# Optimization experiments

Measured on AMD Instinct MI355X. Metric: run time of the kernel, lower is better.

## Reference

```python
import jax, jax.numpy as jnp
import numpy as np

N = 1200          # number of mentions in the block -> NxN SDP matrix
HID = 128         # MLP hidden width
RANK = 64         # Burer-Monteiro factor rank ~ sqrt(2N)
SDP_ITERS = 100   # fixed iteration budget (original caps at 50000)
BN_EPS = 1e-5


def setup_inputs() -> dict:
    key = jax.random.key(0)
    k = jax.random.split(key, 5)
    P = N * (N - 1) // 2
    x = jax.random.normal(k[0], (P, 39), jnp.float32)
    W1 = jax.random.normal(k[1], (39, HID), jnp.float32) * (1.0 / np.sqrt(39.0))
    b1 = jnp.zeros((HID,), jnp.float32)
    gamma = jnp.ones((HID,), jnp.float32)
    beta = jnp.zeros((HID,), jnp.float32)
    W2 = jax.random.normal(k[2], (HID, 1), jnp.float32) * (1.0 / np.sqrt(float(HID)))
    b2 = jnp.zeros((1,), jnp.float32)
    V0 = jax.random.normal(k[3], (N, RANK), jnp.float32)
    return {"x": x, "W1": W1, "b1": b1, "gamma": gamma, "beta": beta,
            "W2": W2, "b2": b2, "V0": V0}


def _forward(x, W1, b1, gamma, beta, W2, b2, V0):
    # MLPLayer: Linear -> BatchNorm (batch stats) -> ReLU -> Linear(->1)
    h = x @ W1 + b1                                   # [P, HID]
    mu = h.mean(axis=0)
    var = h.var(axis=0)
    h = (h - mu) * jax.lax.rsqrt(var + BN_EPS) * gamma + beta
    h = jax.nn.relu(h)
    w = (h @ W2 + b2).reshape(-1)                     # flat edge weights [P]

    # UncompressTransformLayer: flat upper-triangle -> symmetric NxN, zero diag
    iu, ju = jnp.triu_indices(N, k=1)
    A = jnp.zeros((N, N), w.dtype).at[iu, ju].set(w)
    W = A + A.T                                       # [N, N]

    # SDPLayer: max <W, X> s.t. X PSD, diag(X)=1, X>=0 via Burer-Monteiro
    # low-rank factorization with fixed-iteration projected gradient ascent.
    V = V0 / jnp.linalg.norm(V0, axis=1, keepdims=True)
    lr = 1.0 / (jnp.linalg.norm(W) + 1e-8)

    def step(V, _):
        V = V + lr * (W @ V)
        V = V / jnp.linalg.norm(V, axis=1, keepdims=True)
        return V, None

    V, _ = jax.lax.scan(step, V, None, length=SDP_ITERS)
    X = jnp.clip(V @ V.T, 0.0, 1.0)                   # output probabilities [N, N]
    return X


def reference(x, W1, b1, gamma, beta, W2, b2, V0):
    return _forward(x, W1, b1, gamma, beta, W2, b2, V0)
```

## Files before the change

### kernel.cpp

```cpp
#include <hip/hip_runtime.h>

#define NM 1200
#define PP 719400
#define HID 128
#define RANK 64
#define SDP_ITERS 100

#define OFF_S      0
#define OFF_SUMW2  1600
#define OFF_CVEC   1664
#define OFF_W1S    1792
#define OFF_WVEC   6912
#define OFF_WMAT   726400
#define OFF_VA     2166400
#define OFF_VB     2243200

__device__ __forceinline__ float wave_reduce_sum(float v) {
#pragma unroll
    for (int o = 32; o > 0; o >>= 1) v += __shfl_xor(v, o, 64);
    return v;
}

__global__ __launch_bounds__(256) void zero_kernel(float* __restrict__ ws, int n) {
    int i = blockIdx.x * 256 + threadIdx.x;
    if (i < n) ws[i] = 0.0f;
}

#define STATS_BLOCKS 1024
#define KT 40
__global__ __launch_bounds__(256) void stats_kernel(const float* __restrict__ x,
                                                    float* __restrict__ S) {
    __shared__ __align__(8) float tile[KT * 48];
    __shared__ float Sacc[48 * 48];
    const int tid = threadIdx.x;
    for (int i = tid; i < 48 * 48; i += 256) Sacc[i] = 0.f;

    const int rpb = (PP + STATS_BLOCKS - 1) / STATS_BLOCKS;
    const int r0 = blockIdx.x * rpb;
    const int r1 = min(r0 + rpb, PP);

    const int z  = tid >> 6;
    const int ln = tid & 63;
    const int ty = ln >> 3, tx = ln & 7;

    float acc[6][6];
#pragma unroll
    for (int a = 0; a < 6; ++a)
#pragma unroll
        for (int b = 0; b < 6; ++b) acc[a][b] = 0.f;

    for (int t = r0; t < r1; t += KT) {
        const int nr = min(KT, r1 - t);
        __syncthreads();
        const float* xg = x + (size_t)t * 39;
        for (int idx = tid; idx < KT * 48; idx += 256) {
            int rr = idx / 48, cc = idx - rr * 48;
            float v = 0.f;
            if (rr < nr) {
                if (cc < 39) v = xg[rr * 39 + cc];
                else if (cc == 39) v = 1.0f;
            }
            tile[idx] = v;
        }
        __syncthreads();
#pragma unroll 2
        for (int kk = 0; kk < KT / 4; ++kk) {
            const float* row = &tile[(kk * 4 + z) * 48];
            float2 a0 = *(const float2*)(row + ty * 6);
            float2 a1 = *(const float2*)(row + ty * 6 + 2);
            float2 a2 = *(const float2*)(row + ty * 6 + 4);
            float2 b0 = *(const float2*)(row + tx * 6);
            float2 b1 = *(const float2*)(row + tx * 6 + 2);
            float2 b2 = *(const float2*)(row + tx * 6 + 4);
            float av[6] = {a0.x, a0.y, a1.x, a1.y, a2.x, a2.y};
            float bv[6] = {b0.x, b0.y, b1.x, b1.y, b2.x, b2.y};
#pragma unroll
            for (int a = 0; a < 6; ++a)
#pragma unroll
                for (int b = 0; b < 6; ++b)
                    acc[a][b] = fmaf(av[a], bv[b], acc[a][b]);
        }
    }
    __syncthreads();
#pragma unroll
    for (int a = 0; a < 6; ++a)
#pragma unroll
        for (int b = 0; b < 6; ++b)
            atomicAdd(&Sacc[(ty * 6 + a) * 48 + tx * 6 + b], acc[a][b]);
    __syncthreads();
    for (int i = tid; i < 1600; i += 256) {
        int r = i / 40, c = i - r * 40;
        atomicAdd(&S[i], Sacc[r * 48 + c]);
    }
}

__global__ __launch_bounds__(64) void bn_prep(const float* __restrict__ S,
                                              const float* __restrict__ W1,
                                              const float* __restrict__ gamma,
                                              const float* __restrict__ beta,
                                              float* __restrict__ W1s,
                                              float* __restrict__ cvec) {
    const int j = blockIdx.x;
    const int l = threadIdx.x;
    const float invP = 1.0f / (float)PP;
    float q = 0.f;
    for (int idx = l; idx < 39 * 39; idx += 64) {
        int a = idx / 39, b = idx - a * 39;
        q = fmaf(S[a * 40 + b], W1[a * HID + j] * W1[b * HID + j], q);
    }
    float s1 = (l < 39) ? (S[39 * 40 + l] * invP) * W1[l * HID + j] : 0.f;
    q = wave_reduce_sum(q);
    s1 = wave_reduce_sum(s1);
    float var = q * invP - s1 * s1;
    float scale = gamma[j] * (1.0f / sqrtf(var + 1e-5f));
    for (int a = l; a < 39; a += 64) W1s[a * HID + j] = W1[a * HID + j] * scale;
    if (l == 0) cvec[j] = -s1 * scale + beta[j];
}

__global__ __launch_bounds__(256) void mlp_kernel(const float* __restrict__ x,
                                                  const float* __restrict__ W1s,
                                                  const float* __restrict__ cvec,
                                                  const float* __restrict__ W2,
                                                  const float* __restrict__ b2,
                                                  float* __restrict__ w,
                                                  float* __restrict__ sumw2) {
    __shared__ float xt[256 * 39];
    __shared__ float red[4];
    const size_t base = (size_t)blockIdx.x * 256;
    {
        const size_t g0 = base * 39;
        const size_t gmax = (size_t)PP * 39;
        for (int idx = threadIdx.x; idx < 256 * 39; idx += 256) {
            size_t g = g0 + idx;
            xt[idx] = (g < gmax) ? x[g] : 0.f;
        }
    }
    __syncthreads();

    float xr[39];
    {
        const float* xrow = &xt[threadIdx.x * 39];
#pragma unroll
        for (int k = 0; k < 39; ++k) xr[k] = xrow[k];
    }

    float wacc = 0.f;
#pragma unroll 1
    for (int c = 0; c < 2; ++c) {
        float acc[64];
#pragma unroll
        for (int jj = 0; jj < 64; ++jj) acc[jj] = cvec[c * 64 + jj];
#pragma unroll 3
        for (int k = 0; k < 39; ++k) {
            const float xk = xr[k];
            const float* wrow = &W1s[k * HID + c * 64];
#pragma unroll
            for (int jj = 0; jj < 64; ++jj) acc[jj] = fmaf(xk, wrow[jj], acc[jj]);
        }
#pragma unroll
        for (int jj = 0; jj < 64; ++jj)
            wacc = fmaf(fmaxf(acc[jj], 0.f), W2[c * 64 + jj], wacc);
    }

    const size_t p = base + threadIdx.x;
    const float wv = wacc + b2[0];
    float sq = 0.f;
    if (p < (size_t)PP) { w[p] = wv; sq = wv * wv; }
    sq = wave_reduce_sum(sq);
    if ((threadIdx.x & 63) == 0) red[threadIdx.x >> 6] = sq;
    __syncthreads();
    if (threadIdx.x == 0) atomicAdd(sumw2, red[0] + red[1] + red[2] + red[3]);
}

__global__ __launch_bounds__(256) void buildW(const float* __restrict__ w,
                                              float* __restrict__ W) {
    __shared__ float tile[16][17];
    const int bi = blockIdx.y, bj = blockIdx.x;
    if (bi > bj) return;
    const int ty = threadIdx.x >> 4, tx = threadIdx.x & 15;
    const int i = bi * 16 + ty, j = bj * 16 + tx;
    float v = 0.f;
    if (i < j) {
        int p = i * (NM - 1) - (i * (i - 1)) / 2 + (j - i - 1);
        v = w[p];
    }
    tile[ty][tx] = v;
    __syncthreads();
    if (bi == bj) {
        float out = (i < j) ? v : ((i > j) ? tile[tx][ty] : 0.f);
        W[(size_t)i * NM + j] = out;
    } else {
        W[(size_t)i * NM + j] = v;
        W[(size_t)(bj * 16 + ty) * NM + (bi * 16 + tx)] = tile[tx][ty];
    }
}

__global__ __launch_bounds__(256) void v0norm(const float* __restrict__ V0,
                                              float* __restrict__ V) {
    const int i = blockIdx.x * 4 + (threadIdx.x >> 6);
    const int c = threadIdx.x & 63;
    float v = V0[(size_t)i * RANK + c];
    float s = wave_reduce_sum(v * v);
    V[(size_t)i * RANK + c] = v * (1.0f / sqrtf(s));
}

__global__ __launch_bounds__(512) void sdp_step(const float* __restrict__ Vin,
                                                float* __restrict__ Vout,
                                                const float* __restrict__ W,
                                                const float* __restrict__ sumw2) {
    __shared__ float part[8][6][64];
    const int tid = threadIdx.x;
    const int c = tid & 63;
    const int wvid = tid >> 6;
    const int i0 = blockIdx.x * 6;
    const int j0 = __builtin_amdgcn_readfirstlane(wvid * 150);

    const float* __restrict__ Wb = W + (size_t)i0 * NM + j0;
    const float* __restrict__ Vb = Vin + (size_t)j0 * RANK + c;

    float acc[6] = {0.f, 0.f, 0.f, 0.f, 0.f, 0.f};
#pragma unroll 10
    for (int t = 0; t < 150; ++t) {
        const float vc = Vb[(size_t)t * RANK];
#pragma unroll
        for (int r = 0; r < 6; ++r)
            acc[r] = fmaf(Wb[(size_t)r * NM + t], vc, acc[r]);
    }
#pragma unroll
    for (int r = 0; r < 6; ++r) part[wvid][r][c] = acc[r];
    __syncthreads();

    if (tid < 384) {
        const int r2 = tid >> 6, c2 = tid & 63;
        float s = 0.f;
#pragma unroll
        for (int k = 0; k < 8; ++k) s += part[k][r2][c2];
        const float lr = 1.0f / (sqrtf(2.0f * sumw2[0]) + 1e-8f);
        float y = Vin[(size_t)(i0 + r2) * RANK + c2] + lr * s;
        float n = wave_reduce_sum(y * y);
        Vout[(size_t)(i0 + r2) * RANK + c2] = y * (1.0f / sqrtf(n));
    }
}

__global__ __launch_bounds__(256) void vvt_kernel(const float* __restrict__ V,
                                                  float* __restrict__ out) {
    const int bi = blockIdx.y, bj = blockIdx.x;
    if (bi > bj) return;
    __shared__ __align__(16) float Ti[64][132];
    __shared__ __align__(16) float Tj[64][132];
    const int tid = threadIdx.x;
    for (int idx = tid; idx < 128 * 64; idx += 256) {
        int row = idx >> 6, k = idx & 63;
        int gi = bi * 128 + row, gj = bj * 128 + row;
        Ti[k][row] = (gi < NM) ? V[(size_t)gi * RANK + k] : 0.f;
        Tj[k][row] = (gj < NM) ? V[(size_t)gj * RANK + k] : 0.f;
    }
    __syncthreads();
    const int ty = tid >> 4, tx = tid & 15;
    float acc[8][8];
#pragma unroll
    for (int a = 0; a < 8; ++a)
#pragma unroll
        for (int b = 0; b < 8; ++b) acc[a][b] = 0.f;
    for (int k = 0; k < 64; ++k) {
        float4 a0 = *(const float4*)&Ti[k][ty * 8];
        float4 a1 = *(const float4*)&Ti[k][ty * 8 + 4];
        float4 b0 = *(const float4*)&Tj[k][tx * 8];
        float4 b1 = *(const float4*)&Tj[k][tx * 8 + 4];
        float av[8] = {a0.x, a0.y, a0.z, a0.w, a1.x, a1.y, a1.z, a1.w};
        float bv[8] = {b0.x, b0.y, b0.z, b0.w, b1.x, b1.y, b1.z, b1.w};
#pragma unroll
        for (int a = 0; a < 8; ++a)
#pragma unroll
            for (int b = 0; b < 8; ++b)
                acc[a][b] = fmaf(av[a], bv[b], acc[a][b]);
    }
#pragma unroll
    for (int a = 0; a < 8; ++a) {
        int i = bi * 128 + 8 * ty + a;
        if (i >= NM) break;
        int jb = bj * 128 + 8 * tx;
        if (jb + 7 < NM) {
            float4 s0 = {fminf(fmaxf(acc[a][0], 0.f), 1.f), fminf(fmaxf(acc[a][1], 0.f), 1.f),
                         fminf(fmaxf(acc[a][2], 0.f), 1.f), fminf(fmaxf(acc[a][3], 0.f), 1.f)};
            float4 s1 = {fminf(fmaxf(acc[a][4], 0.f), 1.f), fminf(fmaxf(acc[a][5], 0.f), 1.f),
                         fminf(fmaxf(acc[a][6], 0.f), 1.f), fminf(fmaxf(acc[a][7], 0.f), 1.f)};
            *(float4*)&out[(size_t)i * NM + jb] = s0;
            *(float4*)&out[(size_t)i * NM + jb + 4] = s1;
        } else {
#pragma unroll
            for (int b = 0; b < 8; ++b) {
                int j = jb + b;
                if (j < NM) out[(size_t)i * NM + j] = fminf(fmaxf(acc[a][b], 0.f), 1.f);
            }
        }
    }
    if (bi != bj) {
#pragma unroll
        for (int b = 0; b < 8; ++b) {
            int j = bj * 128 + 8 * tx + b;
            if (j >= NM) break;
            int ib = bi * 128 + 8 * ty;
            if (ib + 7 < NM) {
                float4 s0 = {fminf(fmaxf(acc[0][b], 0.f), 1.f), fminf(fmaxf(acc[1][b], 0.f), 1.f),
                             fminf(fmaxf(acc[2][b], 0.f), 1.f), fminf(fmaxf(acc[3][b], 0.f), 1.f)};
                float4 s1 = {fminf(fmaxf(acc[4][b], 0.f), 1.f), fminf(fmaxf(acc[5][b], 0.f), 1.f),
                             fminf(fmaxf(acc[6][b], 0.f), 1.f), fminf(fmaxf(acc[7][b], 0.f), 1.f)};
                *(float4*)&out[(size_t)j * NM + ib] = s0;
                *(float4*)&out[(size_t)j * NM + ib + 4] = s1;
            } else {
#pragma unroll
                for (int a = 0; a < 8; ++a) {
                    int i = ib + a;
                    if (i < NM) out[(size_t)j * NM + i] = fminf(fmaxf(acc[a][b], 0.f), 1.f);
                }
            }
        }
    }
}

extern "C" void kernel_launch(void* const* d_in, const int* in_sizes, int n_in,
                              void* d_out, int out_size, void* d_ws, size_t ws_size,
                              hipStream_t stream) {
    const float* x     = (const float*)d_in[0];
    const float* W1    = (const float*)d_in[1];
    const float* gamma = (const float*)d_in[3];
    const float* beta  = (const float*)d_in[4];
    const float* W2    = (const float*)d_in[5];
    const float* b2    = (const float*)d_in[6];
    const float* V0    = (const float*)d_in[7];
    float* out = (float*)d_out;

    float* ws    = (float*)d_ws;
    float* S     = ws + OFF_S;
    float* sumw2 = ws + OFF_SUMW2;
    float* cvec  = ws + OFF_CVEC;
    float* W1s   = ws + OFF_W1S;
    float* wvec  = ws + OFF_WVEC;
    float* Wmat  = ws + OFF_WMAT;
    float* Va    = ws + OFF_VA;
    float* Vb    = ws + OFF_VB;

    zero_kernel<<<7, 256, 0, stream>>>(ws, OFF_W1S);
    stats_kernel<<<STATS_BLOCKS, 256, 0, stream>>>(x, S);
    bn_prep<<<HID, 64, 0, stream>>>(S, W1, gamma, beta, W1s, cvec);
    mlp_kernel<<<(PP + 255) / 256, 256, 0, stream>>>(x, W1s, cvec, W2, b2, wvec, sumw2);
    buildW<<<dim3(75, 75), 256, 0, stream>>>(wvec, Wmat);
    v0norm<<<NM / 4, 256, 0, stream>>>(V0, Va);
    for (int it = 0; it < SDP_ITERS; ++it) {
        const float* vin = (it & 1) ? Vb : Va;
        float* vout      = (it & 1) ? Va : Vb;
        sdp_step<<<NM / 6, 512, 0, stream>>>(vin, vout, Wmat, sumw2);
    }
    vvt_kernel<<<dim3(10, 10), 256, 0, stream>>>(Va, out);
}
```

Measured before the change: 1.340 ms.

## Restructure SDP step with padded W rows, lane broadcast, and two rows per block

```diff
diff --git a/kernel.cpp b/kernel.cpp
--- a/kernel.cpp
+++ b/kernel.cpp
@@ -1,10 +1,12 @@
 #include <hip/hip_runtime.h>
 
 #define NM 1200
+#define NMP 1280
 #define PP 719400
 #define HID 128
 #define RANK 64
 #define SDP_ITERS 100
+#define STATS_BLOCKS 1024
 
 #define OFF_S      0
 #define OFF_SUMW2  1600
@@ -12,8 +14,9 @@
 #define OFF_W1S    1792
 #define OFF_WVEC   6912
 #define OFF_WMAT   726400
-#define OFF_VA     2166400
-#define OFF_VB     2243200
+#define OFF_VA     2262400
+#define OFF_VB     2344320
+#define OFF_SPART  726400
 
 __device__ __forceinline__ float wave_reduce_sum(float v) {
 #pragma unroll
@@ -21,15 +24,11 @@
     return v;
 }
 
-__global__ __launch_bounds__(256) void zero_kernel(float* __restrict__ ws, int n) {
-    int i = blockIdx.x * 256 + threadIdx.x;
-    if (i < n) ws[i] = 0.0f;
-}
-
-#define STATS_BLOCKS 1024
+__global__ void zero1(float* __restrict__ p) { if (threadIdx.x == 0) p[0] = 0.f; }
+
 #define KT 40
 __global__ __launch_bounds__(256) void stats_kernel(const float* __restrict__ x,
-                                                    float* __restrict__ S) {
+                                                    float* __restrict__ Spart) {
     __shared__ __align__(8) float tile[KT * 48];
     __shared__ float Sacc[48 * 48];
     const int tid = threadIdx.x;
@@ -88,10 +87,25 @@
         for (int b = 0; b < 6; ++b)
             atomicAdd(&Sacc[(ty * 6 + a) * 48 + tx * 6 + b], acc[a][b]);
     __syncthreads();
+    float* out = Spart + (size_t)blockIdx.x * 1600;
     for (int i = tid; i < 1600; i += 256) {
         int r = i / 40, c = i - r * 40;
-        atomicAdd(&S[i], Sacc[r * 48 + c]);
-    }
+        out[i] = Sacc[r * 48 + c];
+    }
+}
+
+__global__ __launch_bounds__(256) void reduce_S(const float* __restrict__ Spart,
+                                                float* __restrict__ S) {
+    const int j = blockIdx.x * 256 + threadIdx.x;
+    if (j >= 1600) return;
+    float s0 = 0.f, s1 = 0.f, s2 = 0.f, s3 = 0.f;
+    for (int b = 0; b < STATS_BLOCKS; b += 4) {
+        s0 += Spart[(size_t)b * 1600 + j];
+        s1 += Spart[(size_t)(b + 1) * 1600 + j];
+        s2 += Spart[(size_t)(b + 2) * 1600 + j];
+        s3 += Spart[(size_t)(b + 3) * 1600 + j];
+    }
+    S[j] = (s0 + s1) + (s2 + s3);
 }
 
 __global__ __launch_bounds__(64) void bn_prep(const float* __restrict__ S,
@@ -117,13 +131,13 @@
     if (l == 0) cvec[j] = -s1 * scale + beta[j];
 }
 
-__global__ __launch_bounds__(256) void mlp_kernel(const float* __restrict__ x,
-                                                  const float* __restrict__ W1s,
-                                                  const float* __restrict__ cvec,
-                                                  const float* __restrict__ W2,
-                                                  const float* __restrict__ b2,
-                                                  float* __restrict__ w,
-                                                  float* __restrict__ sumw2) {
+__global__ __launch_bounds__(256, 1) void mlp_kernel(const float* __restrict__ x,
+                                                     const float* __restrict__ W1s,
+                                                     const float* __restrict__ cvec,
+                                                     const float* __restrict__ W2,
+                                                     const float* __restrict__ b2,
+                                                     float* __restrict__ w,
+                                                     float* __restrict__ sumw2) {
     __shared__ float xt[256 * 39];
     __shared__ float red[4];
     const size_t base = (size_t)blockIdx.x * 256;
@@ -180,18 +194,19 @@
     const int ty = threadIdx.x >> 4, tx = threadIdx.x & 15;
     const int i = bi * 16 + ty, j = bj * 16 + tx;
     float v = 0.f;
-    if (i < j) {
+    if (i < j && j < NM) {
         int p = i * (NM - 1) - (i * (i - 1)) / 2 + (j - i - 1);
         v = w[p];
     }
     tile[ty][tx] = v;
     __syncthreads();
     if (bi == bj) {
-        float out = (i < j) ? v : ((i > j) ? tile[tx][ty] : 0.f);
-        W[(size_t)i * NM + j] = out;
+        float o = (i < j) ? v : ((i > j) ? tile[tx][ty] : 0.f);
+        W[(size_t)i * NMP + j] = o;
     } else {
-        W[(size_t)i * NM + j] = v;
-        W[(size_t)(bj * 16 + ty) * NM + (bi * 16 + tx)] = tile[tx][ty];
+        W[(size_t)i * NMP + j] = v;
+        if (bj < 75)
+            W[(size_t)(bj * 16 + ty) * NMP + (bi * 16 + tx)] = tile[tx][ty];
     }
 }
 
@@ -204,41 +219,50 @@
     V[(size_t)i * RANK + c] = v * (1.0f / sqrtf(s));
 }
 
-__global__ __launch_bounds__(512) void sdp_step(const float* __restrict__ Vin,
+__global__ __launch_bounds__(256) void sdp_step(const float* __restrict__ Vin,
                                                 float* __restrict__ Vout,
                                                 const float* __restrict__ W,
                                                 const float* __restrict__ sumw2) {
-    __shared__ float part[8][6][64];
+    __shared__ float part[4][2][64];
     const int tid = threadIdx.x;
     const int c = tid & 63;
-    const int wvid = tid >> 6;
-    const int i0 = blockIdx.x * 6;
-    const int j0 = __builtin_amdgcn_readfirstlane(wvid * 150);
-
-    const float* __restrict__ Wb = W + (size_t)i0 * NM + j0;
-    const float* __restrict__ Vb = Vin + (size_t)j0 * RANK + c;
-
-    float acc[6] = {0.f, 0.f, 0.f, 0.f, 0.f, 0.f};
-#pragma unroll 10
-    for (int t = 0; t < 150; ++t) {
-        const float vc = Vb[(size_t)t * RANK];
-#pragma unroll
-        for (int r = 0; r < 6; ++r)
-            acc[r] = fmaf(Wb[(size_t)r * NM + t], vc, acc[r]);
-    }
-#pragma unroll
-    for (int r = 0; r < 6; ++r) part[wvid][r][c] = acc[r];
-    __syncthreads();
-
-    if (tid < 384) {
-        const int r2 = tid >> 6, c2 = tid & 63;
-        float s = 0.f;
-#pragma unroll
-        for (int k = 0; k < 8; ++k) s += part[k][r2][c2];
+    const int kq = tid >> 6;
+    const int i0 = blockIdx.x * 2;
+    const float* __restrict__ W0 = W + (size_t)i0 * NMP;
+    const float* __restrict__ W1 = W0 + NMP;
+
+    float a0 = 0.f, a1 = 0.f, b0 = 0.f, b1 = 0.f;
+    const int kbase = kq * 320;
+#pragma unroll 1
+    for (int g = 0; g < 5; ++g) {
+        const int k0 = kbase + g * 64;
+        const int w0i = __float_as_int(W0[k0 + c]);
+        const int w1i = __float_as_int(W1[k0 + c]);
+        const float* __restrict__ vp = Vin + (size_t)k0 * RANK + c;
+#pragma unroll
+        for (int t = 0; t < 64; t += 2) {
+            float va = vp[(size_t)t * RANK];
+            float vb = vp[(size_t)(t + 1) * RANK];
+            float s0a = __int_as_float(__builtin_amdgcn_readlane(w0i, t));
+            float s1a = __int_as_float(__builtin_amdgcn_readlane(w1i, t));
+            float s0b = __int_as_float(__builtin_amdgcn_readlane(w0i, t + 1));
+            float s1b = __int_as_float(__builtin_amdgcn_readlane(w1i, t + 1));
+            a0 = fmaf(s0a, va, a0);
+            a1 = fmaf(s1a, va, a1);
+            b0 = fmaf(s0b, vb, b0);
+            b1 = fmaf(s1b, vb, b1);
+        }
+    }
+    part[kq][0][c] = a0 + b0;
+    part[kq][1][c] = a1 + b1;
+    __syncthreads();
+    if (tid < 128) {
+        const int r = tid >> 6, c2 = tid & 63;
+        float s = part[0][r][c2] + part[1][r][c2] + part[2][r][c2] + part[3][r][c2];
         const float lr = 1.0f / (sqrtf(2.0f * sumw2[0]) + 1e-8f);
-        float y = Vin[(size_t)(i0 + r2) * RANK + c2] + lr * s;
+        float y = Vin[(size_t)(i0 + r) * RANK + c2] + lr * s;
         float n = wave_reduce_sum(y * y);
-        Vout[(size_t)(i0 + r2) * RANK + c2] = y * (1.0f / sqrtf(n));
+        Vout[(size_t)(i0 + r) * RANK + c2] = y * (1.0f / sqrtf(n));
     }
 }
 
@@ -340,17 +364,19 @@
     float* Wmat  = ws + OFF_WMAT;
     float* Va    = ws + OFF_VA;
     float* Vb    = ws + OFF_VB;
-
-    zero_kernel<<<7, 256, 0, stream>>>(ws, OFF_W1S);
-    stats_kernel<<<STATS_BLOCKS, 256, 0, stream>>>(x, S);
+    float* Spart = ws + OFF_SPART;
+
+    zero1<<<1, 64, 0, stream>>>(sumw2);
+    stats_kernel<<<STATS_BLOCKS, 256, 0, stream>>>(x, Spart);
+    reduce_S<<<7, 256, 0, stream>>>(Spart, S);
     bn_prep<<<HID, 64, 0, stream>>>(S, W1, gamma, beta, W1s, cvec);
     mlp_kernel<<<(PP + 255) / 256, 256, 0, stream>>>(x, W1s, cvec, W2, b2, wvec, sumw2);
-    buildW<<<dim3(75, 75), 256, 0, stream>>>(wvec, Wmat);
+    buildW<<<dim3(80, 75), 256, 0, stream>>>(wvec, Wmat);
     v0norm<<<NM / 4, 256, 0, stream>>>(V0, Va);
     for (int it = 0; it < SDP_ITERS; ++it) {
         const float* vin = (it & 1) ? Vb : Va;
         float* vout      = (it & 1) ? Va : Vb;
-        sdp_step<<<NM / 6, 512, 0, stream>>>(vin, vout, Wmat, sumw2);
+        sdp_step<<<NM / 2, 256, 0, stream>>>(vin, vout, Wmat, sumw2);
     }
     vvt_kernel<<<dim3(10, 10), 256, 0, stream>>>(Va, out);
 }
```

After: 1.716 ms. 1.28x slower.
